# Kernel tuning notes

Hardware: AMD Instinct MI355X
Metric: run time of the kernel (lower is better)

The kernel has to match this reference:

```python
import math
import jax, jax.numpy as jnp
import numpy as np

NQ = 10      # n_qubits
NB = 4       # n_blocks (angle encoding layers)
VD = 6       # vqc_depth (hardware-efficient layers)
LAT = 128    # latent_dim
NOBS = 9     # n_qubits - k_local + 1 sliding 2-local groups
DIM = 2 ** NQ


def sin_embed(t, dim):
    half = dim // 2
    freqs = jnp.exp(-math.log(10000.0) * jnp.arange(half, dtype=jnp.float32) / half)
    args = t[:, None] * freqs[None, :]
    return jnp.concatenate([jnp.cos(args), jnp.sin(args)], axis=-1)


def apply_ry(psi, theta, q):
    # psi: [B, 2^NQ] complex; theta: scalar or [B]
    B = psi.shape[0]
    p = psi.reshape(B, 2 ** q, 2, 2 ** (NQ - 1 - q))
    th = jnp.broadcast_to(theta, (B,))
    c = jnp.cos(th / 2)[:, None, None].astype(psi.dtype)
    s = jnp.sin(th / 2)[:, None, None].astype(psi.dtype)
    p0, p1 = p[:, :, 0, :], p[:, :, 1, :]
    return jnp.stack([c * p0 - s * p1, s * p0 + c * p1], axis=2).reshape(B, -1)


def apply_cnot(psi, ctrl, tgt):
    B = psi.shape[0]
    pt = psi.reshape((B,) + (2,) * NQ)
    p0 = jax.lax.index_in_dim(pt, 0, axis=ctrl + 1, keepdims=True)
    p1 = jnp.flip(jax.lax.index_in_dim(pt, 1, axis=ctrl + 1, keepdims=True), axis=tgt + 1)
    return jnp.concatenate([p0, p1], axis=ctrl + 1).reshape(B, -1)


def run_circuit(enc, var_params):
    B = enc.shape[0]
    psi = jnp.zeros((B, DIM), dtype=jnp.complex64).at[:, 0].set(1.0)
    # angle encoding: RY data re-uploading blocks with CNOT ladders between blocks
    for layer in range(NB):
        for q in range(NQ):
            psi = apply_ry(psi, enc[:, layer * NQ + q], q)
        if layer < NB - 1:
            for q in range(0, NQ - 1, 2):
                psi = apply_cnot(psi, q, q + 1)
            for q in range(1, NQ - 1, 2):
                psi = apply_cnot(psi, q, q + 1)
    # hardware-efficient variational layers
    for ly in range(VD):
        for q in range(NQ):
            psi = apply_ry(psi, var_params[ly, q], q)
        for q in range(0, NQ - 1, 2):
            psi = apply_cnot(psi, q, q + 1)
        for q in range(1, NQ - 1, 2):
            psi = apply_cnot(psi, q, q + 1)
    return psi


def build_H(A_p, B_p, D_p):
    # create_Hermitian: lower-tri (row-major) = A + iB; h[i-1,i-1] = D[i]; H = h + h^dagger
    r, c = np.tril_indices(4, -1)  # order matches count+j loop: (1,0),(2,0),(2,1),(3,0),(3,1),(3,2)
    L = jnp.zeros((NOBS, 4, 4), dtype=jnp.complex64)
    L = L.at[:, r, c].set(A_p.astype(jnp.complex64) + 1j * B_p.astype(jnp.complex64))
    d = 2.0 * jnp.concatenate([D_p[:, 1:4], jnp.zeros((NOBS, 1), dtype=D_p.dtype)], axis=1)
    H = L + jnp.conj(jnp.swapaxes(L, 1, 2))
    H = H + jax.vmap(jnp.diag)(d).astype(jnp.complex64)
    return H


def expvals(psi, H):
    B = psi.shape[0]
    outs = []
    for s in range(NOBS):  # sliding window [s, s+1]
        pg = psi.reshape(B, 2 ** s, 4, 2 ** (NQ - s - 2))
        outs.append(jnp.einsum('balr,lk,bakr->b', jnp.conj(pg), H[s], pg).real)
    return jnp.stack(outs, axis=-1)


def setup_inputs() -> dict:
    ks = jax.random.split(jax.random.key(0), 12)
    B = 2048
    return {
        'z_t': jax.random.normal(ks[0], (B, LAT), dtype=jnp.float32),
        't': jax.random.uniform(ks[1], (B,), dtype=jnp.float32),
        'W1': 0.05 * jax.random.normal(ks[2], (2 * LAT, 256), dtype=jnp.float32),
        'b1': jnp.zeros((256,), dtype=jnp.float32),
        'W2': 0.05 * jax.random.normal(ks[3], (256, NB * NQ), dtype=jnp.float32),
        'b2': jnp.zeros((NB * NQ,), dtype=jnp.float32),
        'var_params': 0.01 * jax.random.normal(ks[4], (VD, NQ), dtype=jnp.float32),
        'A_p': 2.0 * jax.random.normal(ks[5], (NOBS, 6), dtype=jnp.float32),
        'B_p': 2.0 * jax.random.normal(ks[6], (NOBS, 6), dtype=jnp.float32),
        'D_p': 2.0 * jax.random.normal(ks[7], (NOBS, 4), dtype=jnp.float32),
        'W3': 0.05 * jax.random.normal(ks[8], (NOBS, 256), dtype=jnp.float32),
        'b3': jnp.zeros((256,), dtype=jnp.float32),
        'W4': 0.05 * jax.random.normal(ks[9], (256, LAT), dtype=jnp.float32),
        'b4': jnp.zeros((LAT,), dtype=jnp.float32),
    }


def reference(z_t, t, W1, b1, W2, b2, var_params, A_p, B_p, D_p, W3, b3, W4, b4):
    x = jnp.concatenate([z_t, sin_embed(t, LAT)], axis=-1)   # [B, 2*LAT]
    h = jax.nn.silu(x @ W1 + b1)
    enc = h @ W2 + b2                                         # [B, NB*NQ]
    psi = run_circuit(enc, var_params)                        # [B, 2^NQ]
    obs = expvals(psi, build_H(A_p, B_p, D_p))                # [B, NOBS]
    return jax.nn.silu(obs @ W3 + b3) @ W4 + b4               # [B, LAT]
```

## Files before the change

### kernel.cpp

```cpp
#include <hip/hip_runtime.h>
#include <math.h>

#define NOBS 9

typedef float f2 __attribute__((ext_vector_type(2)));

__device__ __forceinline__ float silu_f(float x) { return x / (1.f + expf(-x)); }
__device__ __forceinline__ f2 splat2(float x) { return (f2){x, x}; }
__device__ __forceinline__ f2 fma2(f2 a, f2 b, f2 c) { return __builtin_elementwise_fma(a, b, c); }

template<int CTRL>
__device__ __forceinline__ float dpp_perm(float x) {
  return __int_as_float(__builtin_amdgcn_update_dpp(0, __float_as_int(x), CTRL, 0xF, 0xF, true));
}
template<int PAT>
__device__ __forceinline__ float ds_swz(float x) {
  return __int_as_float(__builtin_amdgcn_ds_swizzle(__float_as_int(x), PAT));
}
__device__ __forceinline__ float x4f(float x) { return ds_swz<0x101F>(x); }

__device__ __forceinline__ float wave_sum(float x) {
  x += dpp_perm<0xB1>(x);
  x += dpp_perm<0x4E>(x);
  x += x4f(x);
  x += dpp_perm<0x128>(x);
  x += ds_swz<0x401F>(x);
  x += __shfl_xor(x, 32, 64);
  return x;
}

template<int M>
__device__ __forceinline__ void ry_reg(float v[16], float c, float s) {
#pragma unroll
  for (int r = 0; r < 16; ++r) {
    if ((r & M) == 0) {
      float p0 = v[r], p1 = v[r | M];
      v[r]     = c * p0 - s * p1;
      v[r | M] = s * p0 + c * p1;
    }
  }
}

__device__ __forceinline__ void apply_rys(float v[16], int lane,
                                          const float* __restrict__ cc,
                                          const float* __restrict__ ss) {
  ry_reg<8>(v, cc[0], ss[0]);
  ry_reg<4>(v, cc[1], ss[1]);
  ry_reg<2>(v, cc[2], ss[2]);
  ry_reg<1>(v, cc[3], ss[3]);
  { float c = cc[4], s = ss[4], sp = (lane & 32) ? s : -s;
#pragma unroll
    for (int r = 0; r < 16; ++r) { float p = __shfl_xor(v[r], 32, 64); v[r] = fmaf(c, v[r], sp * p); } }
  { float c = cc[5], s = ss[5], sp = (lane & 16) ? s : -s;
#pragma unroll
    for (int r = 0; r < 16; ++r) { float p = __shfl_xor(v[r], 16, 64); v[r] = fmaf(c, v[r], sp * p); } }
  { float c = cc[6], s = ss[6], sp = (lane & 8) ? s : -s;
#pragma unroll
    for (int r = 0; r < 16; ++r) { float p = dpp_perm<0x128>(v[r]); v[r] = fmaf(c, v[r], sp * p); } }
  { float c = cc[7], s = ss[7], sp = (lane & 4) ? s : -s;
#pragma unroll
    for (int r = 0; r < 16; ++r) { float p = x4f(v[r]); v[r] = fmaf(c, v[r], sp * p); } }
  { float c = cc[8], s = ss[8], sp = (lane & 2) ? s : -s;
#pragma unroll
    for (int r = 0; r < 16; ++r) { float p = dpp_perm<0x4E>(v[r]); v[r] = fmaf(c, v[r], sp * p); } }
  { float c = cc[9], s = ss[9], sp = (lane & 1) ? s : -s;
#pragma unroll
    for (int r = 0; r < 16; ++r) { float p = dpp_perm<0xB1>(v[r]); v[r] = fmaf(c, v[r], sp * p); } }
}

__device__ __forceinline__ void cnot_ladder(float v[16], int lane) {
  float t;
  t=v[8];  v[8]=v[12];  v[12]=t;
  t=v[9];  v[9]=v[13];  v[13]=t;
  t=v[10]; v[10]=v[14]; v[14]=t;
  t=v[11]; v[11]=v[15]; v[15]=t;
  t=v[2];  v[2]=v[3];   v[3]=t;
  t=v[6];  v[6]=v[7];   v[7]=t;
  t=v[10]; v[10]=v[11]; v[11]=t;
  t=v[14]; v[14]=v[15]; v[15]=t;
  int se = lane ^ ((lane & 42) >> 1);
#pragma unroll
  for (int r = 0; r < 16; ++r) v[r] = __shfl(v[r], se, 64);
  t=v[4];  v[4]=v[6];   v[6]=t;
  t=v[5];  v[5]=v[7];   v[7]=t;
  t=v[12]; v[12]=v[14]; v[14]=t;
  t=v[13]; v[13]=v[15]; v[15]=t;
  int so  = lane ^ ((lane & 20) >> 1);
  int so1 = so ^ 32;
#pragma unroll
  for (int r = 0; r < 16; ++r) v[r] = __shfl(v[r], (r & 1) ? so1 : so, 64);
}

__global__ __launch_bounds__(64) void varcs_kernel(const float* __restrict__ varp,
                                                   float* __restrict__ varc,
                                                   float* __restrict__ vars) {
  int tid = threadIdx.x;
  if (tid < 60) {
    float s, c;
    sincosf(0.5f * varp[tid], &s, &c);
    varc[tid] = c;
    vars[tid] = s;
  }
}

__global__ __launch_bounds__(256) void enc_kernel(
    const float* __restrict__ z, const float* __restrict__ t,
    const float* __restrict__ W1, const float* __restrict__ b1,
    const float* __restrict__ W2, const float* __restrict__ b2,
    float* __restrict__ csg, float* __restrict__ sng) {
  __shared__ __align__(16) float4 xs4[256];
  __shared__ float hs[4][256];
  int tid = threadIdx.x;
  int b0 = blockIdx.x * 4;

  if (tid < 128) {
    xs4[tid] = (float4){z[(b0 + 0) * 128 + tid], z[(b0 + 1) * 128 + tid],
                        z[(b0 + 2) * 128 + tid], z[(b0 + 3) * 128 + tid]};
  } else {
    int i = tid - 128, j = i & 63;
    float freq = expf(-9.2103403719761836f * (float)j * (1.f / 64.f));
    float a0 = t[b0] * freq, a1 = t[b0 + 1] * freq, a2 = t[b0 + 2] * freq, a3 = t[b0 + 3] * freq;
    xs4[tid] = (i < 64) ? (float4){cosf(a0), cosf(a1), cosf(a2), cosf(a3)}
                        : (float4){sinf(a0), sinf(a1), sinf(a2), sinf(a3)};
  }
  __syncthreads();

  {
    f2 a01 = splat2(b1[tid]), a23 = a01;
#pragma unroll 8
    for (int k = 0; k < 256; ++k) {
      float wv = W1[k * 256 + tid];
      float4 x = xs4[k];
      a01 = fma2((f2){x.x, x.y}, splat2(wv), a01);
      a23 = fma2((f2){x.z, x.w}, splat2(wv), a23);
    }
    hs[0][tid] = silu_f(a01.x);
    hs[1][tid] = silu_f(a01.y);
    hs[2][tid] = silu_f(a23.x);
    hs[3][tid] = silu_f(a23.y);
  }
  __syncthreads();

  if (tid < 160) {
    int r = tid / 40, c = tid - r * 40;
    float acc = b2[c];
#pragma unroll 8
    for (int k = 0; k < 256; ++k)
      acc = fmaf(hs[r][k], W2[k * 40 + c], acc);
    float s, cv;
    sincosf(0.5f * acc, &s, &cv);
    csg[(b0 + r) * 40 + c] = cv;
    sng[(b0 + r) * 40 + c] = s;
  }
}

__global__ __launch_bounds__(64) void circuit_kernel(
    const float* __restrict__ csg, const float* __restrict__ sng,
    const float* __restrict__ varc, const float* __restrict__ vars,
    const float* __restrict__ A_p, const float* __restrict__ D_p,
    float* __restrict__ obs) {
  __shared__ float sw[1024];
  int lane = threadIdx.x;
  int b = blockIdx.x;
  const float* cc = csg + b * 40;
  const float* ss = sng + b * 40;

  float base = 1.f;
  base *= (lane & 32) ? ss[4] : cc[4];
  base *= (lane & 16) ? ss[5] : cc[5];
  base *= (lane & 8)  ? ss[6] : cc[6];
  base *= (lane & 4)  ? ss[7] : cc[7];
  base *= (lane & 2)  ? ss[8] : cc[8];
  base *= (lane & 1)  ? ss[9] : cc[9];
  float v[16];
#pragma unroll
  for (int r = 0; r < 16; ++r) {
    float p = base;
    p *= (r & 8) ? ss[0] : cc[0];
    p *= (r & 4) ? ss[1] : cc[1];
    p *= (r & 2) ? ss[2] : cc[2];
    p *= (r & 1) ? ss[3] : cc[3];
    v[r] = p;
  }
  cnot_ladder(v, lane);
#pragma unroll 1
  for (int layer = 1; layer < 4; ++layer) {
    apply_rys(v, lane, cc + layer * 10, ss + layer * 10);
    if (layer < 3) cnot_ladder(v, lane);
  }
#pragma unroll 1
  for (int ly = 0; ly < 6; ++ly) {
    apply_rys(v, lane, varc + ly * 10, vars + ly * 10);
    cnot_ladder(v, lane);
  }

#pragma unroll
  for (int r = 0; r < 16; ++r) sw[r * 64 + lane] = v[r];

#pragma unroll 1
  for (int s = 0; s < NOBS; ++s) {
    const int r8 = 8 - s;
    const int stride = 1 << r8;
    float h10 = A_p[s*6+0], h20 = A_p[s*6+1], h21 = A_p[s*6+2];
    float h30 = A_p[s*6+3], h31 = A_p[s*6+4], h32 = A_p[s*6+5];
    float d0 = 2.f * D_p[s*4+1], d1 = 2.f * D_p[s*4+2], d2 = 2.f * D_p[s*4+3];
    float acc = 0.f;
#pragma unroll
    for (int k = 0; k < 4; ++k) {
      int p = lane + 64 * k;
      int a  = p >> r8;
      int rr = p & (stride - 1);
      int bse = (a << (r8 + 2)) + rr;
      float x0 = sw[bse];
      float x1 = sw[bse + stride];
      float x2 = sw[bse + 2 * stride];
      float x3 = sw[bse + 3 * stride];
      acc += d0 * x0 * x0 + d1 * x1 * x1 + d2 * x2 * x2
           + 2.f * (h10 * x1 * x0 + h20 * x2 * x0 + h21 * x2 * x1
                  + h30 * x3 * x0 + h31 * x3 * x1 + h32 * x3 * x2);
    }
    acc = wave_sum(acc);
    if (lane == 0) obs[b * NOBS + s] = acc;
  }
}

__global__ __launch_bounds__(256) void head_kernel(
    const float* __restrict__ obs, const float* __restrict__ W3,
    const float* __restrict__ b3, const float* __restrict__ W4,
    const float* __restrict__ b4, float* __restrict__ out) {
  __shared__ float os[4][NOBS];
  __shared__ __align__(16) float4 hp4[256];
  int tid = threadIdx.x;
  int b0 = blockIdx.x * 4;

  if (tid < 4 * NOBS) os[tid / NOBS][tid % NOBS] = obs[b0 * NOBS + tid];
  __syncthreads();

  {
    f2 q01 = splat2(b3[tid]), q23 = q01;
#pragma unroll
    for (int s = 0; s < NOBS; ++s) {
      float wv = W3[s * 256 + tid];
      q01 = fma2((f2){os[0][s], os[1][s]}, splat2(wv), q01);
      q23 = fma2((f2){os[2][s], os[3][s]}, splat2(wv), q23);
    }
    hp4[tid] = (float4){silu_f(q01.x), silu_f(q01.y), silu_f(q23.x), silu_f(q23.y)};
  }
  __syncthreads();

  {
    int c = tid & 127, rg = tid >> 7;
    f2 acc = splat2(b4[c]);
#pragma unroll 8
    for (int k = 0; k < 256; ++k) {
      float wv = W4[k * 128 + c];
      float4 h = hp4[k];
      f2 hp = (rg == 0) ? (f2){h.x, h.y} : (f2){h.z, h.w};
      acc = fma2(hp, splat2(wv), acc);
    }
    out[(b0 + 2 * rg) * 128 + c]     = acc.x;
    out[(b0 + 2 * rg + 1) * 128 + c] = acc.y;
  }
}


extern "C" void kernel_launch(void* const* d_in, const int* in_sizes, int n_in,
                              void* d_out, int out_size, void* d_ws, size_t ws_size,
                              hipStream_t stream) {
  const float* z_t  = (const float*)d_in[0];
  const float* t    = (const float*)d_in[1];
  const float* W1   = (const float*)d_in[2];
  const float* b1   = (const float*)d_in[3];
  const float* W2   = (const float*)d_in[4];
  const float* b2   = (const float*)d_in[5];
  const float* varp = (const float*)d_in[6];
  const float* A_p  = (const float*)d_in[7];
  const float* D_p  = (const float*)d_in[9];
  const float* W3   = (const float*)d_in[10];
  const float* b3   = (const float*)d_in[11];
  const float* W4   = (const float*)d_in[12];
  const float* b4   = (const float*)d_in[13];
  float* out = (float*)d_out;

  int B = in_sizes[1];

  float* csg  = (float*)d_ws;
  float* sng  = csg + (size_t)B * 40;
  float* obs  = sng + (size_t)B * 40;
  float* varc = obs + (size_t)B * 9;
  float* vars = varc + 64;

  varcs_kernel<<<1, 64, 0, stream>>>(varp, varc, vars);
  enc_kernel<<<B / 4, 256, 0, stream>>>(z_t, t, W1, b1, W2, b2, csg, sng);
  circuit_kernel<<<B, 64, 0, stream>>>(csg, sng, varc, vars, A_p, D_p, obs);
  head_kernel<<<B / 4, 256, 0, stream>>>(obs, W3, b3, W4, b4, out);
}
```

Before: 140.7 us.

## Fuse encoder, circuit, and head into one kernel with staggered weight traversal

Merges the four separate launches (variational sincos, encoder MLP, circuit simulation, head MLP) into a single 256-thread kernel that handles four batch rows per block. Each wave simulates one row's circuit, and all intermediates stay in shared memory. This removes launch overhead and the global round-trips for cos/sin angles and observables. It also offsets each block's starting k index in the weight loops so concurrent blocks read different rows of W1, W2 and W4 instead of hammering the same ones. In exchange, shared memory per block and register pressure rise, which may lower occupancy for the circuit phase.

```diff
diff --git a/kernel.cpp b/kernel.cpp
--- a/kernel.cpp
+++ b/kernel.cpp
@@ -91,27 +91,35 @@
   for (int r = 0; r < 16; ++r) v[r] = __shfl(v[r], (r & 1) ? so1 : so, 64);
 }
 
-__global__ __launch_bounds__(64) void varcs_kernel(const float* __restrict__ varp,
-                                                   float* __restrict__ varc,
-                                                   float* __restrict__ vars) {
+
+__global__ __launch_bounds__(256) void fused_kernel(
+    const float* __restrict__ z, const float* __restrict__ t,
+    const float* __restrict__ W1, const float* __restrict__ b1,
+    const float* __restrict__ W2, const float* __restrict__ b2,
+    const float* __restrict__ varp,
+    const float* __restrict__ A_p, const float* __restrict__ D_p,
+    const float* __restrict__ W3, const float* __restrict__ b3,
+    const float* __restrict__ W4, const float* __restrict__ b4,
+    float* __restrict__ out) {
+  __shared__ __align__(16) float4 xs4[256];
+  __shared__ float hs[4][256];
+  __shared__ float dump[4][1024];
+  __shared__ float cs[4][40], sn[4][40];
+  __shared__ float vcs[64], vsn[64];
+  __shared__ float os[4][NOBS];
+  __shared__ __align__(16) float4 hp4[256];
+
   int tid = threadIdx.x;
+  int b0 = blockIdx.x * 4;
+  int wave = tid >> 6;
+  int lane = tid & 63;
+  int koff = (((blockIdx.x << 2) | wave) * 53) & 255;
+
   if (tid < 60) {
     float s, c;
     sincosf(0.5f * varp[tid], &s, &c);
-    varc[tid] = c;
-    vars[tid] = s;
-  }
-}
-
-__global__ __launch_bounds__(256) void enc_kernel(
-    const float* __restrict__ z, const float* __restrict__ t,
-    const float* __restrict__ W1, const float* __restrict__ b1,
-    const float* __restrict__ W2, const float* __restrict__ b2,
-    float* __restrict__ csg, float* __restrict__ sng) {
-  __shared__ __align__(16) float4 xs4[256];
-  __shared__ float hs[4][256];
-  int tid = threadIdx.x;
-  int b0 = blockIdx.x * 4;
+    vcs[tid] = c; vsn[tid] = s;
+  }
 
   if (tid < 128) {
     xs4[tid] = (float4){z[(b0 + 0) * 128 + tid], z[(b0 + 1) * 128 + tid],
@@ -128,7 +136,8 @@
   {
     f2 a01 = splat2(b1[tid]), a23 = a01;
 #pragma unroll 8
-    for (int k = 0; k < 256; ++k) {
+    for (int j = 0; j < 256; ++j) {
+      int k = (koff + j) & 255;
       float wv = W1[k * 256 + tid];
       float4 x = xs4[k];
       a01 = fma2((f2){x.x, x.y}, splat2(wv), a01);
@@ -145,95 +154,79 @@
     int r = tid / 40, c = tid - r * 40;
     float acc = b2[c];
 #pragma unroll 8
-    for (int k = 0; k < 256; ++k)
+    for (int j = 0; j < 256; ++j) {
+      int k = (koff + j) & 255;
       acc = fmaf(hs[r][k], W2[k * 40 + c], acc);
+    }
     float s, cv;
     sincosf(0.5f * acc, &s, &cv);
-    csg[(b0 + r) * 40 + c] = cv;
-    sng[(b0 + r) * 40 + c] = s;
-  }
-}
-
-__global__ __launch_bounds__(64) void circuit_kernel(
-    const float* __restrict__ csg, const float* __restrict__ sng,
-    const float* __restrict__ varc, const float* __restrict__ vars,
-    const float* __restrict__ A_p, const float* __restrict__ D_p,
-    float* __restrict__ obs) {
-  __shared__ float sw[1024];
-  int lane = threadIdx.x;
-  int b = blockIdx.x;
-  const float* cc = csg + b * 40;
-  const float* ss = sng + b * 40;
-
-  float base = 1.f;
-  base *= (lane & 32) ? ss[4] : cc[4];
-  base *= (lane & 16) ? ss[5] : cc[5];
-  base *= (lane & 8)  ? ss[6] : cc[6];
-  base *= (lane & 4)  ? ss[7] : cc[7];
-  base *= (lane & 2)  ? ss[8] : cc[8];
-  base *= (lane & 1)  ? ss[9] : cc[9];
-  float v[16];
-#pragma unroll
-  for (int r = 0; r < 16; ++r) {
-    float p = base;
-    p *= (r & 8) ? ss[0] : cc[0];
-    p *= (r & 4) ? ss[1] : cc[1];
-    p *= (r & 2) ? ss[2] : cc[2];
-    p *= (r & 1) ? ss[3] : cc[3];
-    v[r] = p;
-  }
-  cnot_ladder(v, lane);
+    cs[r][c] = cv; sn[r][c] = s;
+  }
+  __syncthreads();
+
+  {
+    const float* cc = cs[wave];
+    const float* ss = sn[wave];
+
+    float base = 1.f;
+    base *= (lane & 32) ? ss[4] : cc[4];
+    base *= (lane & 16) ? ss[5] : cc[5];
+    base *= (lane & 8)  ? ss[6] : cc[6];
+    base *= (lane & 4)  ? ss[7] : cc[7];
+    base *= (lane & 2)  ? ss[8] : cc[8];
+    base *= (lane & 1)  ? ss[9] : cc[9];
+    float v[16];
+#pragma unroll
+    for (int r = 0; r < 16; ++r) {
+      float p = base;
+      p *= (r & 8) ? ss[0] : cc[0];
+      p *= (r & 4) ? ss[1] : cc[1];
+      p *= (r & 2) ? ss[2] : cc[2];
+      p *= (r & 1) ? ss[3] : cc[3];
+      v[r] = p;
+    }
+    cnot_ladder(v, lane);
 #pragma unroll 1
-  for (int layer = 1; layer < 4; ++layer) {
-    apply_rys(v, lane, cc + layer * 10, ss + layer * 10);
-    if (layer < 3) cnot_ladder(v, lane);
-  }
+    for (int layer = 1; layer < 4; ++layer) {
+      apply_rys(v, lane, cc + layer * 10, ss + layer * 10);
+      if (layer < 3) cnot_ladder(v, lane);
+    }
 #pragma unroll 1
-  for (int ly = 0; ly < 6; ++ly) {
-    apply_rys(v, lane, varc + ly * 10, vars + ly * 10);
-    cnot_ladder(v, lane);
-  }
-
-#pragma unroll
-  for (int r = 0; r < 16; ++r) sw[r * 64 + lane] = v[r];
+    for (int ly = 0; ly < 6; ++ly) {
+      apply_rys(v, lane, vcs + ly * 10, vsn + ly * 10);
+      cnot_ladder(v, lane);
+    }
+
+    float* sw = dump[wave];
+#pragma unroll
+    for (int r = 0; r < 16; ++r) sw[r * 64 + lane] = v[r];
 
 #pragma unroll 1
-  for (int s = 0; s < NOBS; ++s) {
-    const int r8 = 8 - s;
-    const int stride = 1 << r8;
-    float h10 = A_p[s*6+0], h20 = A_p[s*6+1], h21 = A_p[s*6+2];
-    float h30 = A_p[s*6+3], h31 = A_p[s*6+4], h32 = A_p[s*6+5];
-    float d0 = 2.f * D_p[s*4+1], d1 = 2.f * D_p[s*4+2], d2 = 2.f * D_p[s*4+3];
-    float acc = 0.f;
-#pragma unroll
-    for (int k = 0; k < 4; ++k) {
-      int p = lane + 64 * k;
-      int a  = p >> r8;
-      int rr = p & (stride - 1);
-      int bse = (a << (r8 + 2)) + rr;
-      float x0 = sw[bse];
-      float x1 = sw[bse + stride];
-      float x2 = sw[bse + 2 * stride];
-      float x3 = sw[bse + 3 * stride];
-      acc += d0 * x0 * x0 + d1 * x1 * x1 + d2 * x2 * x2
-           + 2.f * (h10 * x1 * x0 + h20 * x2 * x0 + h21 * x2 * x1
-                  + h30 * x3 * x0 + h31 * x3 * x1 + h32 * x3 * x2);
-    }
-    acc = wave_sum(acc);
-    if (lane == 0) obs[b * NOBS + s] = acc;
-  }
-}
-
-__global__ __launch_bounds__(256) void head_kernel(
-    const float* __restrict__ obs, const float* __restrict__ W3,
-    const float* __restrict__ b3, const float* __restrict__ W4,
-    const float* __restrict__ b4, float* __restrict__ out) {
-  __shared__ float os[4][NOBS];
-  __shared__ __align__(16) float4 hp4[256];
-  int tid = threadIdx.x;
-  int b0 = blockIdx.x * 4;
-
-  if (tid < 4 * NOBS) os[tid / NOBS][tid % NOBS] = obs[b0 * NOBS + tid];
+    for (int s = 0; s < NOBS; ++s) {
+      const int r8 = 8 - s;
+      const int stride = 1 << r8;
+      float h10 = A_p[s*6+0], h20 = A_p[s*6+1], h21 = A_p[s*6+2];
+      float h30 = A_p[s*6+3], h31 = A_p[s*6+4], h32 = A_p[s*6+5];
+      float d0 = 2.f * D_p[s*4+1], d1 = 2.f * D_p[s*4+2], d2 = 2.f * D_p[s*4+3];
+      float acc = 0.f;
+#pragma unroll
+      for (int k = 0; k < 4; ++k) {
+        int p = lane + 64 * k;
+        int a  = p >> r8;
+        int rr = p & (stride - 1);
+        int bse = (a << (r8 + 2)) + rr;
+        float x0 = sw[bse];
+        float x1 = sw[bse + stride];
+        float x2 = sw[bse + 2 * stride];
+        float x3 = sw[bse + 3 * stride];
+        acc += d0 * x0 * x0 + d1 * x1 * x1 + d2 * x2 * x2
+             + 2.f * (h10 * x1 * x0 + h20 * x2 * x0 + h21 * x2 * x1
+                    + h30 * x3 * x0 + h31 * x3 * x1 + h32 * x3 * x2);
+      }
+      acc = wave_sum(acc);
+      if (lane == 0) os[wave][s] = acc;
+    }
+  }
   __syncthreads();
 
   {
@@ -252,10 +245,11 @@
     int c = tid & 127, rg = tid >> 7;
     f2 acc = splat2(b4[c]);
 #pragma unroll 8
-    for (int k = 0; k < 256; ++k) {
+    for (int j = 0; j < 256; ++j) {
+      int k = (koff + j) & 255;
       float wv = W4[k * 128 + c];
       float4 h = hp4[k];
-      f2 hp = (rg == 0) ? (f2){h.x, h.y} : (f2){h.z, h.w};
+      f2 hp = rg ? (f2){h.z, h.w} : (f2){h.x, h.y};
       acc = fma2(hp, splat2(wv), acc);
     }
     out[(b0 + 2 * rg) * 128 + c]     = acc.x;
@@ -284,14 +278,6 @@
 
   int B = in_sizes[1];
 
-  float* csg  = (float*)d_ws;
-  float* sng  = csg + (size_t)B * 40;
-  float* obs  = sng + (size_t)B * 40;
-  float* varc = obs + (size_t)B * 9;
-  float* vars = varc + 64;
-
-  varcs_kernel<<<1, 64, 0, stream>>>(varp, varc, vars);
-  enc_kernel<<<B / 4, 256, 0, stream>>>(z_t, t, W1, b1, W2, b2, csg, sng);
-  circuit_kernel<<<B, 64, 0, stream>>>(csg, sng, varc, vars, A_p, D_p, obs);
-  head_kernel<<<B / 4, 256, 0, stream>>>(obs, W3, b3, W4, b4, out);
-}
+  fused_kernel<<<B / 4, 256, 0, stream>>>(z_t, t, W1, b1, W2, b2, varp,
+                                          A_p, D_p, W3, b3, W4, b4, out);
+}
```

After: 130.1 us. -7.5%, faster.
